# Optimization experiments

Measured on AMD Instinct MI355X. Metric: run time of the kernel, lower is better.

Reference implementation:

```python
import jax, jax.numpy as jnp
import numpy as np

B, S, H, NH = 1, 4096, 768, 12
D = H // NH  # per-head dim = 64


def setup_inputs() -> dict:
    key = jax.random.key(0)
    ks = jax.random.split(key, 10)
    p = 0.02  # param scale
    return {
        "x": jax.random.normal(ks[0], (B, S, H), jnp.float32),
        "Wq": jax.random.normal(ks[1], (H, H), jnp.float32) * p,
        "bq": jax.random.normal(ks[2], (H,), jnp.float32) * p,
        "Wk": jax.random.normal(ks[3], (H, H), jnp.float32) * p,
        "bk": jax.random.normal(ks[4], (H,), jnp.float32) * p,
        "Wv": jax.random.normal(ks[5], (H, H), jnp.float32) * p,
        "bv": jax.random.normal(ks[6], (H,), jnp.float32) * p,
        "Wo": jax.random.normal(ks[7], (H, H), jnp.float32) * p,
        "bo": jax.random.normal(ks[8], (H,), jnp.float32) * p,
        "attn_mask": jax.random.randint(ks[9], (B, 1, 1, S), 0, 2).astype(bool),
    }


def _split_heads(t):
    # [B, S, H] -> [B, NH, S, D]
    return t.reshape(B, S, NH, D).transpose(0, 2, 1, 3)


def reference(x, Wq, bq, Wk, bk, Wv, bv, Wo, bo, attn_mask):
    q = _split_heads(x @ Wq.T + bq)
    k = _split_heads(x @ Wk.T + bk)
    v = _split_heads(x @ Wv.T + bv)
    scores = jnp.einsum('bhqd,bhkd->bhqk', q, k) / np.sqrt(D).astype(np.float32)
    scores = jnp.where(attn_mask, jnp.float32(-1e9), scores)
    attn = jax.nn.softmax(scores, axis=-1)
    ctx = jnp.einsum('bhqk,bhkd->bhqd', attn, v)
    ctx = ctx.transpose(0, 2, 1, 3).reshape(B, S, H)  # merge heads
    return ctx @ Wo.T + bo
```

## Files before the change

### kernel.cpp

```cpp
#include <hip/hip_runtime.h>
#include <stdint.h>

#define S_LEN 4096
#define HDIM  768
#define NHEAD 12
#define DHEAD 64

typedef _Float16 f16;
typedef __attribute__((ext_vector_type(8)))  _Float16 f16x8;
typedef __attribute__((ext_vector_type(4)))  _Float16 f16x4;
typedef __attribute__((ext_vector_type(4)))  float    f32x4;
typedef __attribute__((ext_vector_type(16))) float    f32x16;

typedef __attribute__((address_space(1))) void gv_t;
typedef __attribute__((address_space(3))) void lv_t;

__device__ __forceinline__ void async_copy16(const void* g, void* l) {
  __builtin_amdgcn_global_load_lds((gv_t*)g, (lv_t*)l, 16, 0, 0);
}

__device__ __forceinline__ float fast_exp2(float x) {
#if __has_builtin(__builtin_amdgcn_exp2f)
  return __builtin_amdgcn_exp2f(x);
#else
  return exp2f(x);
#endif
}

__device__ __forceinline__ int swz4(int row) { return (row ^ (row >> 2)) & 3; }

constexpr size_t OFF_META = 0;
constexpr size_t OFF_RIDX = 256;
constexpr size_t OFF_XB   = 65536;
constexpr size_t SZ_XB    = (size_t)S_LEN * HDIM * 2;
constexpr size_t OFF_WQKV = OFF_XB + SZ_XB;
constexpr size_t SZ_WQKV  = (size_t)3 * HDIM * HDIM * 2;
constexpr size_t OFF_WO   = OFF_WQKV + SZ_WQKV;
constexpr size_t SZ_WO    = (size_t)HDIM * HDIM * 2;
constexpr size_t OFF_Q    = OFF_WO + SZ_WO;
constexpr size_t SZ_HD    = (size_t)NHEAD * S_LEN * DHEAD * 2;
constexpr size_t OFF_K    = OFF_Q + SZ_HD;
constexpr size_t OFF_VT   = OFF_K + SZ_HD;
constexpr size_t OFF_PO   = OFF_VT + SZ_HD;

__global__ __launch_bounds__(256) void k_prep(const float* __restrict__ x,
                                              const float* __restrict__ wq,
                                              const float* __restrict__ wk,
                                              const float* __restrict__ wv,
                                              const float* __restrict__ wo,
                                              const int* __restrict__ mi,
                                              f16* __restrict__ dst,
                                              int* __restrict__ ridx,
                                              int* __restrict__ meta) {
  __shared__ int s_flag;
  __shared__ int s_cnt[256];
  const int b = blockIdx.x, tid = threadIdx.x;
  if (b < 5376) {
    int i = b * 256 + tid;
    const float* src; int off;
    if (i < 786432) { src = x; off = i; }
    else {
      int j = i - 786432;
      int w = j / 147456;
      off = j - w * 147456;
      src = (w == 0) ? wq : (w == 1) ? wk : (w == 2) ? wv : wo;
    }
    float4 v = ((const float4*)src)[off];
    f16x4 h;
    h[0] = (f16)v.x; h[1] = (f16)v.y; h[2] = (f16)v.z; h[3] = (f16)v.w;
    ((f16x4*)dst)[i] = h;
    return;
  }
  if (tid == 0) s_flag = 1;
  __syncthreads();
  int bad = 0;
  #pragma unroll
  for (int k = 0; k < 4; ++k) {
    int v = mi[k * 256 + tid];
    if (v != 0 && v != 1) bad = 1;
  }
  if (bad) atomicAnd(&s_flag, 0);
  __syncthreads();
  const int isInt = s_flag;
  const unsigned char* mu8 = (const unsigned char*)mi;
  int keep[16]; int cnt = 0;
  const int s0 = tid * 16;
  #pragma unroll
  for (int k = 0; k < 16; ++k) {
    int mval = isInt ? mi[s0 + k] : (int)mu8[s0 + k];
    keep[k] = (mval == 0) ? 1 : 0;
    cnt += keep[k];
    ridx[s0 + k] = 0;
  }
  s_cnt[tid] = cnt;
  __syncthreads();
  for (int off = 1; off < 256; off <<= 1) {
    int t = (tid >= off) ? s_cnt[tid - off] : 0;
    __syncthreads();
    s_cnt[tid] += t;
    __syncthreads();
  }
  int base = s_cnt[tid] - cnt;
  #pragma unroll
  for (int k = 0; k < 16; ++k) {
    if (keep[k]) { ridx[base] = s0 + k; ++base; }
  }
  if (tid == 255) meta[0] = s_cnt[255];
}

__global__ __launch_bounds__(256) void k_qkv(
    const f16* __restrict__ xb, const f16* __restrict__ wqkv,
    const float* __restrict__ bq, const float* __restrict__ bk, const float* __restrict__ bv,
    const int* __restrict__ ridx, const int* __restrict__ meta,
    f16* __restrict__ Qh, f16* __restrict__ Kc, f16* __restrict__ Vtc) {
  __shared__ __attribute__((aligned(16))) f16 lA[128 * 32];
  __shared__ __attribute__((aligned(16))) f16 lB[128 * 32];
  __shared__ __attribute__((aligned(16))) f16 lT[64 * 132];
  const int tid = threadIdx.x;
  const int wid = tid >> 6, lane = tid & 63;
  const int hf = lane >> 5, l31 = lane & 31;
  const int wm = wid >> 1, wn = wid & 1;
  const int tn = blockIdx.x;
  const int m0 = blockIdx.y * 128;
  const int mat = tn / 6;
  const int nb = (tn % 6) * 128;
  const int kc = meta[0];
  const int kcp = (kc + 63) & ~63;
  if (mat != 0 && m0 >= kc) return;
  const f16* wbase = wqkv + (size_t)mat * HDIM * HDIM;

  const int ar0 = tid >> 2, ar1 = 64 + (tid >> 2);
  const f16* asrc0;
  const f16* asrc1;
  if (mat == 0) {
    asrc0 = xb + (size_t)(m0 + ar0) * HDIM;
    asrc1 = xb + (size_t)(m0 + ar1) * HDIM;
  } else {
    int g0 = (m0 + ar0 < kc) ? ridx[m0 + ar0] : 0;
    int g1 = (m0 + ar1 < kc) ? ridx[m0 + ar1] : 0;
    asrc0 = xb + (size_t)g0 * HDIM;
    asrc1 = xb + (size_t)g1 * HDIM;
  }
  const int slot = tid & 3;
  const int gs0 = slot ^ swz4(ar0);
  const int gs1 = slot ^ swz4(ar1);

  f32x16 acc[2][2] = {};

  for (int k0 = 0; k0 < HDIM; k0 += 32) {
    async_copy16((const char*)(asrc0 + k0) + gs0 * 16, (char*)lA + (wid * 64) * 16);
    async_copy16((const char*)(asrc1 + k0) + gs1 * 16, (char*)lA + (256 + wid * 64) * 16);
    async_copy16((const char*)(wbase + (size_t)(nb + ar0) * HDIM + k0) + gs0 * 16,
                 (char*)lB + (wid * 64) * 16);
    async_copy16((const char*)(wbase + (size_t)(nb + ar1) * HDIM + k0) + gs1 * 16,
                 (char*)lB + (256 + wid * 64) * 16);
    __syncthreads();
    #pragma unroll
    for (int kk = 0; kk < 2; ++kk) {
      f16x8 af[2], bf[2];
      #pragma unroll
      for (int mi = 0; mi < 2; ++mi) {
        int row = wm * 64 + mi * 32 + l31;
        af[mi] = *(const f16x8*)&lA[row * 32 + (((kk * 2 + hf) ^ swz4(row)) * 8)];
      }
      #pragma unroll
      for (int ni = 0; ni < 2; ++ni) {
        int row = wn * 64 + ni * 32 + l31;
        bf[ni] = *(const f16x8*)&lB[row * 32 + (((kk * 2 + hf) ^ swz4(row)) * 8)];
      }
      #pragma unroll
      for (int mi = 0; mi < 2; ++mi)
        #pragma unroll
        for (int ni = 0; ni < 2; ++ni)
          acc[mi][ni] = __builtin_amdgcn_mfma_f32_32x32x16_f16(af[mi], bf[ni], acc[mi][ni], 0, 0, 0);
    }
    __syncthreads();
  }

  if (mat == 2) {
    const float* bias = bv;
    #pragma unroll
    for (int pass = 0; pass < 2; ++pass) {
      __syncthreads();
      if (wn == pass) {
        #pragma unroll
        for (int ni = 0; ni < 2; ++ni) {
          const int n = nb + wn * 64 + ni * 32 + l31;
          const float bn = bias[n];
          const int dloc = ni * 32 + l31;
          #pragma unroll
          for (int mi = 0; mi < 2; ++mi) {
            #pragma unroll
            for (int rg = 0; rg < 4; ++rg) {
              const int sbase = wm * 64 + mi * 32 + 8 * rg + 4 * hf;
              f16x4 v4;
              #pragma unroll
              for (int j = 0; j < 4; ++j) {
                const int s = m0 + sbase + j;
                v4[j] = (s < kc) ? (f16)(acc[mi][ni][rg * 4 + j] + bn) : (f16)0.f;
              }
              *(f16x4*)&lT[dloc * 132 + sbase] = v4;
            }
          }
        }
      }
      __syncthreads();
      const int headg = (nb >> 6) + pass;
      for (int u = tid; u < 1024; u += 256) {
        const int d = u >> 4, p8 = u & 15;
        const int base16 = (p8 >> 1) * 16, half = p8 & 1;
        f16x4 lo = *(const f16x4*)&lT[d * 132 + base16 + half * 4];
        f16x4 hi = *(const f16x4*)&lT[d * 132 + base16 + 8 + half * 4];
        f16x8 o;
        o[0] = lo[0]; o[1] = lo[1]; o[2] = lo[2]; o[3] = lo[3];
        o[4] = hi[0]; o[5] = hi[1]; o[6] = hi[2]; o[7] = hi[3];
        *(f16x8*)&Vtc[((size_t)headg * DHEAD + d) * S_LEN + m0 + p8 * 8] = o;
      }
    }
    return;
  }

  const float* bias = (mat == 0) ? bq : bk;
  const float qscale = 0.125f * 1.44269504088896341f;
  #pragma unroll
  for (int mi = 0; mi < 2; ++mi) {
    #pragma unroll
    for (int ni = 0; ni < 2; ++ni) {
      int n = nb + wn * 64 + ni * 32 + l31;
      int head = n >> 6, d = n & 63;
      float b = bias[n];
      #pragma unroll
      for (int reg = 0; reg < 16; ++reg) {
        int s = m0 + wm * 64 + mi * 32 + (reg & 3) + 8 * (reg >> 2) + 4 * hf;
        float val = acc[mi][ni][reg] + b;
        if (mat == 0) {
          Qh[((size_t)head * S_LEN + s) * DHEAD + d] = (f16)(val * qscale);
        } else if (s < kc) {
          Kc[((size_t)head * S_LEN + s) * DHEAD + d] = (f16)val;
        } else if (s < kcp) {
          Kc[((size_t)head * S_LEN + s) * DHEAD + d] = (f16)0.f;
        }
      }
    }
  }
}

__global__ __launch_bounds__(128, 2) void k_attn(
    const f16* __restrict__ Qh, const f16* __restrict__ Kc, const f16* __restrict__ Vtc,
    const int* __restrict__ meta, f16* __restrict__ PO) {
  __shared__ __attribute__((aligned(16))) f16 lK[2][64 * 64];
  __shared__ __attribute__((aligned(16))) f16 lV[2][64 * 64];
  __shared__ float lil[64];
  const int tid = threadIdx.x;
  const int wid = tid >> 6, lane = tid & 63;
  const int hf = lane >> 5, l31 = lane & 31, r7 = l31 & 7;

  const int lid = blockIdx.x;
  const int w = ((lid & 7) * 96) + (lid >> 3);
  const int head = w >> 6;
  const int q0 = (w & 63) * 64 + wid * 32;

  const int kc = meta[0];
  const int nkt = (kc + 63) >> 6;

  const f16* Qp = Qh + ((size_t)head * S_LEN + q0 + l31) * DHEAD;
  f16x8 qf[4];
  #pragma unroll
  for (int dc = 0; dc < 4; ++dc) qf[dc] = *(const f16x8*)(Qp + dc * 16 + hf * 8);

  f32x16 accO[2] = {};
  float ls0 = 0.f, ls1 = 0.f, ls2 = 0.f, ls3 = 0.f;

  const char* kbase = (const char*)(Kc + (size_t)head * S_LEN * DHEAD);
  const char* vbase = (const char*)(Vtc + (size_t)head * DHEAD * S_LEN);

  const int crow = tid >> 3, cslot = tid & 7;
  const int gsc = cslot ^ (crow & 7);

  auto stage = [&](int t, int buf) {
    const int j0 = t * 64;
    #pragma unroll
    for (int it = 0; it < 4; ++it) {
      const int row = it * 16 + crow;
      async_copy16(kbase + (size_t)(j0 + row) * 128 + gsc * 16,
                   (char*)&lK[buf][0] + (it * 128 + wid * 64) * 16);
      async_copy16(vbase + (size_t)row * (S_LEN * 2) + (size_t)j0 * 2 + gsc * 16,
                   (char*)&lV[buf][0] + (it * 128 + wid * 64) * 16);
    }
  };

  int cur = 0;
  stage(0, 0);
  __syncthreads();

  for (int t = 0; t < nkt; ++t) {
    const bool more = (t + 1 < nkt);
    if (more) stage(t + 1, cur ^ 1);

    f16x8 af0[4], af1[4];
    #pragma unroll
    for (int dc = 0; dc < 4; ++dc) {
      af0[dc] = *(const f16x8*)&lK[cur][l31 * 64 + ((((dc << 1) | hf) ^ r7) * 8)];
      af1[dc] = *(const f16x8*)&lK[cur][(32 + l31) * 64 + ((((dc << 1) | hf) ^ r7) * 8)];
    }
    f32x16 sA = {}, sB = {};
    #pragma unroll
    for (int dc = 0; dc < 4; ++dc) {
      sA = __builtin_amdgcn_mfma_f32_32x32x16_f16(af0[dc], qf[dc], sA, 0, 0, 0);
      sB = __builtin_amdgcn_mfma_f32_32x32x16_f16(af1[dc], qf[dc], sB, 0, 0, 0);
    }

    f16x8 pfA[2];
    #pragma unroll
    for (int u = 0; u < 16; ++u) {
      sA[u] = fast_exp2(sA[u]);
      if (u & 1) ls1 += sA[u]; else ls0 += sA[u];
    }
    #pragma unroll
    for (int cc = 0; cc < 2; ++cc)
      #pragma unroll
      for (int u = 0; u < 8; ++u) pfA[cc][u] = (f16)sA[8 * cc + u];

    #pragma unroll
    for (int cc = 0; cc < 2; ++cc) {
      #pragma unroll
      for (int dh = 0; dh < 2; ++dh) {
        const int vrow = dh * 32 + l31;
        f16x8 vf = *(const f16x8*)&lV[cur][vrow * 64 + ((((cc << 1) | hf) ^ r7) * 8)];
        accO[dh] = __builtin_amdgcn_mfma_f32_32x32x16_f16(pfA[cc], vf, accO[dh], 0, 0, 0);
      }
    }

    f16x8 pfB[2];
    #pragma unroll
    for (int u = 0; u < 16; ++u) {
      sB[u] = fast_exp2(sB[u]);
      if (u & 1) ls3 += sB[u]; else ls2 += sB[u];
    }
    #pragma unroll
    for (int cc = 0; cc < 2; ++cc)
      #pragma unroll
      for (int u = 0; u < 8; ++u) pfB[cc][u] = (f16)sB[8 * cc + u];

    #pragma unroll
    for (int cc = 0; cc < 2; ++cc) {
      #pragma unroll
      for (int dh = 0; dh < 2; ++dh) {
        const int vrow = dh * 32 + l31;
        f16x8 vf = *(const f16x8*)&lV[cur][vrow * 64 + (((((2 + cc) << 1) | hf) ^ r7) * 8)];
        accO[dh] = __builtin_amdgcn_mfma_f32_32x32x16_f16(pfB[cc], vf, accO[dh], 0, 0, 0);
      }
    }

    if (more) {
      __syncthreads();
      cur ^= 1;
    }
  }

  float lsum = (ls0 + ls1) + (ls2 + ls3);
  lsum += __shfl_xor(lsum, 32);
  lsum -= (float)(nkt * 64 - kc);
  if (hf == 0) lil[wid * 32 + l31] = 1.0f / lsum;
  __syncthreads();

  f16* ost = (f16*)lK + wid * 2048;
  #pragma unroll
  for (int dh = 0; dh < 2; ++dh)
    #pragma unroll
    for (int reg = 0; reg < 16; ++reg) {
      int row = (reg & 3) + 8 * (reg >> 2) + 4 * hf;
      ost[row * 64 + dh * 32 + l31] = (f16)(accO[dh][reg] * lil[wid * 32 + row]);
    }
  #pragma unroll
  for (int p = 0; p < 4; ++p) {
    int row = p * 8 + (lane >> 3), sl = lane & 7;
    f16x8 v = *(const f16x8*)&ost[row * 64 + sl * 8];
    *(f16x8*)&PO[((size_t)head * S_LEN + q0 + row) * DHEAD + sl * 8] = v;
  }
}

__global__ __launch_bounds__(256) void k_out(
    const f16* __restrict__ PO, const f16* __restrict__ wo,
    const float* __restrict__ bo, float* __restrict__ out) {
  __shared__ __attribute__((aligned(16))) f16 lA[128 * 64];
  __shared__ __attribute__((aligned(16))) f16 lB[64 * 64];
  const int tid = threadIdx.x;
  const int wid = tid >> 6, lane = tid & 63;
  const int hf = lane >> 5, l31 = lane & 31;
  const int wm = wid >> 1, wn = wid & 1;
  const int lid = blockIdx.x;
  const int w = ((lid & 7) * 48) + (lid >> 3);
  const int nb = (w % 12) * 64;
  const int m0 = (w / 12) * 128;

  f32x16 acc[2] = {};

  for (int head = 0; head < NHEAD; ++head) {
    #pragma unroll
    for (int it = 0; it < 4; ++it) {
      int c = it * 256 + tid;
      int row = c >> 3, slot = c & 7;
      int gs = slot ^ (row & 7);
      async_copy16((const char*)(PO + ((size_t)head * S_LEN + m0 + row) * DHEAD) + gs * 16,
                   (char*)lA + (it * 256 + wid * 64) * 16);
    }
    #pragma unroll
    for (int it = 0; it < 2; ++it) {
      int c = it * 256 + tid;
      int row = c >> 3, slot = c & 7;
      int gs = slot ^ (row & 7);
      async_copy16((const char*)(wo + (size_t)(nb + row) * HDIM + head * 64) + gs * 16,
                   (char*)lB + (it * 256 + wid * 64) * 16);
    }
    __syncthreads();
    #pragma unroll
    for (int kk = 0; kk < 4; ++kk) {
      f16x8 af[2], bf;
      #pragma unroll
      for (int mi = 0; mi < 2; ++mi) {
        int row = wm * 64 + mi * 32 + l31;
        af[mi] = *(const f16x8*)&lA[row * 64 + ((((kk << 1) | hf) ^ (row & 7)) * 8)];
      }
      int rb = wn * 32 + l31;
      bf = *(const f16x8*)&lB[rb * 64 + ((((kk << 1) | hf) ^ (rb & 7)) * 8)];
      #pragma unroll
      for (int mi = 0; mi < 2; ++mi)
        acc[mi] = __builtin_amdgcn_mfma_f32_32x32x16_f16(af[mi], bf, acc[mi], 0, 0, 0);
    }
    __syncthreads();
  }

  const int n = nb + wn * 32 + l31;
  const float b = bo[n];
  #pragma unroll
  for (int mi = 0; mi < 2; ++mi) {
    #pragma unroll
    for (int reg = 0; reg < 16; ++reg) {
      int s = m0 + wm * 64 + mi * 32 + (reg & 3) + 8 * (reg >> 2) + 4 * hf;
      out[(size_t)s * HDIM + n] = acc[mi][reg] + b;
    }
  }
}

extern "C" void kernel_launch(void* const* d_in, const int* in_sizes, int n_in,
                              void* d_out, int out_size, void* d_ws, size_t ws_size,
                              hipStream_t stream) {
  const float* x  = (const float*)d_in[0];
  const float* Wq = (const float*)d_in[1];
  const float* bq = (const float*)d_in[2];
  const float* Wk = (const float*)d_in[3];
  const float* bk = (const float*)d_in[4];
  const float* Wv = (const float*)d_in[5];
  const float* bv = (const float*)d_in[6];
  const float* Wo = (const float*)d_in[7];
  const float* bo = (const float*)d_in[8];
  const int*   mask = (const int*)d_in[9];
  float* out = (float*)d_out;

  char* ws = (char*)d_ws;
  int* meta  = (int*)(ws + OFF_META);
  int* ridx  = (int*)(ws + OFF_RIDX);
  f16* xb    = (f16*)(ws + OFF_XB);
  f16* wqkv  = (f16*)(ws + OFF_WQKV);
  f16* wob   = (f16*)(ws + OFF_WO);
  f16* Qh    = (f16*)(ws + OFF_Q);
  f16* Kc    = (f16*)(ws + OFF_K);
  f16* Vtc   = (f16*)(ws + OFF_VT);
  f16* PO    = (f16*)(ws + OFF_PO);

  k_prep<<<dim3(5377), 256, 0, stream>>>(x, Wq, Wk, Wv, Wo, mask, xb, ridx, meta);
  k_qkv<<<dim3(18, 32), 256, 0, stream>>>(xb, wqkv, bq, bk, bv, ridx, meta, Qh, Kc, Vtc);
  k_attn<<<dim3(768), 128, 0, stream>>>(Qh, Kc, Vtc, meta, PO);
  k_out<<<dim3(384), 256, 0, stream>>>(PO, wob, bo, out);
}
```

Baseline: 168.9 us.

## Software-pipeline attention loop with triple-buffered K/V and lookahead QK MFMA

Expands K/V shared-memory staging to three buffers, prefetching two tiles ahead. It also computes the next tile's QK^T scores while the current tile's exponentials and PV products run. The aim is to hide MFMA and exp latency and reduce stalls at barriers. The cost is more LDS per block and higher register pressure from keeping two score tiles live.

Result: slower. 173.3 us (+2.6%).

```diff
diff --git a/kernel.cpp b/kernel.cpp
--- a/kernel.cpp
+++ b/kernel.cpp
@@ -248,8 +248,8 @@
 __global__ __launch_bounds__(128, 2) void k_attn(
     const f16* __restrict__ Qh, const f16* __restrict__ Kc, const f16* __restrict__ Vtc,
     const int* __restrict__ meta, f16* __restrict__ PO) {
-  __shared__ __attribute__((aligned(16))) f16 lK[2][64 * 64];
-  __shared__ __attribute__((aligned(16))) f16 lV[2][64 * 64];
+  __shared__ __attribute__((aligned(16))) f16 lK[3][64 * 64];
+  __shared__ __attribute__((aligned(16))) f16 lV[3][64 * 64];
   __shared__ float lil[64];
   const int tid = threadIdx.x;
   const int wid = tid >> 6, lane = tid & 63;
@@ -289,73 +289,80 @@
     }
   };
 
+  f32x16 sA = {}, sB = {};
+  stage(0, 0);
+  if (nkt > 1) stage(1, 1);
+  __syncthreads();
+  {
+    f16x8 a0[4], a1[4];
+    #pragma unroll
+    for (int dc = 0; dc < 4; ++dc) {
+      a0[dc] = *(const f16x8*)&lK[0][l31 * 64 + ((((dc << 1) | hf) ^ r7) * 8)];
+      a1[dc] = *(const f16x8*)&lK[0][(32 + l31) * 64 + ((((dc << 1) | hf) ^ r7) * 8)];
+    }
+    #pragma unroll
+    for (int dc = 0; dc < 4; ++dc) {
+      sA = __builtin_amdgcn_mfma_f32_32x32x16_f16(a0[dc], qf[dc], sA, 0, 0, 0);
+      sB = __builtin_amdgcn_mfma_f32_32x32x16_f16(a1[dc], qf[dc], sB, 0, 0, 0);
+    }
+  }
+
   int cur = 0;
-  stage(0, 0);
-  __syncthreads();
-
   for (int t = 0; t < nkt; ++t) {
     const bool more = (t + 1 < nkt);
-    if (more) stage(t + 1, cur ^ 1);
-
-    f16x8 af0[4], af1[4];
-    #pragma unroll
-    for (int dc = 0; dc < 4; ++dc) {
-      af0[dc] = *(const f16x8*)&lK[cur][l31 * 64 + ((((dc << 1) | hf) ^ r7) * 8)];
-      af1[dc] = *(const f16x8*)&lK[cur][(32 + l31) * 64 + ((((dc << 1) | hf) ^ r7) * 8)];
-    }
-    f32x16 sA = {}, sB = {};
-    #pragma unroll
-    for (int dc = 0; dc < 4; ++dc) {
-      sA = __builtin_amdgcn_mfma_f32_32x32x16_f16(af0[dc], qf[dc], sA, 0, 0, 0);
-      sB = __builtin_amdgcn_mfma_f32_32x32x16_f16(af1[dc], qf[dc], sB, 0, 0, 0);
-    }
-
-    f16x8 pfA[2];
+    const int nxt = (cur == 2) ? 0 : cur + 1;
+    const int nn2 = (nxt == 2) ? 0 : nxt + 1;
+    if (t + 2 < nkt) stage(t + 2, nn2);
+
+    f16x8 a0[4], a1[4];
+    if (more) {
+      #pragma unroll
+      for (int dc = 0; dc < 4; ++dc) {
+        a0[dc] = *(const f16x8*)&lK[nxt][l31 * 64 + ((((dc << 1) | hf) ^ r7) * 8)];
+        a1[dc] = *(const f16x8*)&lK[nxt][(32 + l31) * 64 + ((((dc << 1) | hf) ^ r7) * 8)];
+      }
+    }
+
+    f16x8 pfA[2], pfB[2];
     #pragma unroll
     for (int u = 0; u < 16; ++u) {
       sA[u] = fast_exp2(sA[u]);
-      if (u & 1) ls1 += sA[u]; else ls0 += sA[u];
+      sB[u] = fast_exp2(sB[u]);
+      if (u & 1) { ls1 += sA[u]; ls3 += sB[u]; }
+      else       { ls0 += sA[u]; ls2 += sB[u]; }
     }
     #pragma unroll
     for (int cc = 0; cc < 2; ++cc)
       #pragma unroll
-      for (int u = 0; u < 8; ++u) pfA[cc][u] = (f16)sA[8 * cc + u];
+      for (int u = 0; u < 8; ++u) {
+        pfA[cc][u] = (f16)sA[8 * cc + u];
+        pfB[cc][u] = (f16)sB[8 * cc + u];
+      }
+
+    f32x16 nA = {}, nB = {};
+    if (more) {
+      #pragma unroll
+      for (int dc = 0; dc < 4; ++dc) {
+        nA = __builtin_amdgcn_mfma_f32_32x32x16_f16(a0[dc], qf[dc], nA, 0, 0, 0);
+        nB = __builtin_amdgcn_mfma_f32_32x32x16_f16(a1[dc], qf[dc], nB, 0, 0, 0);
+      }
+    }
 
     #pragma unroll
     for (int cc = 0; cc < 2; ++cc) {
       #pragma unroll
       for (int dh = 0; dh < 2; ++dh) {
         const int vrow = dh * 32 + l31;
-        f16x8 vf = *(const f16x8*)&lV[cur][vrow * 64 + ((((cc << 1) | hf) ^ r7) * 8)];
-        accO[dh] = __builtin_amdgcn_mfma_f32_32x32x16_f16(pfA[cc], vf, accO[dh], 0, 0, 0);
-      }
-    }
-
-    f16x8 pfB[2];
-    #pragma unroll
-    for (int u = 0; u < 16; ++u) {
-      sB[u] = fast_exp2(sB[u]);
-      if (u & 1) ls3 += sB[u]; else ls2 += sB[u];
-    }
-    #pragma unroll
-    for (int cc = 0; cc < 2; ++cc)
-      #pragma unroll
-      for (int u = 0; u < 8; ++u) pfB[cc][u] = (f16)sB[8 * cc + u];
-
-    #pragma unroll
-    for (int cc = 0; cc < 2; ++cc) {
-      #pragma unroll
-      for (int dh = 0; dh < 2; ++dh) {
-        const int vrow = dh * 32 + l31;
-        f16x8 vf = *(const f16x8*)&lV[cur][vrow * 64 + (((((2 + cc) << 1) | hf) ^ r7) * 8)];
-        accO[dh] = __builtin_amdgcn_mfma_f32_32x32x16_f16(pfB[cc], vf, accO[dh], 0, 0, 0);
-      }
-    }
-
-    if (more) {
-      __syncthreads();
-      cur ^= 1;
-    }
+        f16x8 vf0 = *(const f16x8*)&lV[cur][vrow * 64 + ((((cc << 1) | hf) ^ r7) * 8)];
+        f16x8 vf1 = *(const f16x8*)&lV[cur][vrow * 64 + (((((2 + cc) << 1) | hf) ^ r7) * 8)];
+        accO[dh] = __builtin_amdgcn_mfma_f32_32x32x16_f16(pfA[cc], vf0, accO[dh], 0, 0, 0);
+        accO[dh] = __builtin_amdgcn_mfma_f32_32x32x16_f16(pfB[cc], vf1, accO[dh], 0, 0, 0);
+      }
+    }
+
+    if (more) __syncthreads();
+    sA = nA; sB = nB;
+    cur = nxt;
   }
 
   float lsum = (ls0 + ls1) + (ls2 + ls3);
```
